# Optimization experiments

Measured on AMD Instinct MI355X. Metric: run time of the kernel, lower is better.

The kernel has to match this reference:

```python
import jax, jax.numpy as jnp
import numpy as np

N, E, D, H = 100000, 1600000, 128, 4
HD = D // H  # per-head dim


def setup_inputs() -> dict:
    key = jax.random.key(0)
    ks = jax.random.split(key, 16)
    s = 1.0 / np.sqrt(D)
    inp = {
        "x": jax.random.normal(ks[0], (N, D), jnp.float32),
        "edge_index": jax.random.randint(ks[1], (2, E), 0, N, jnp.int64),
        # GCNConv params
        "w_gcn": jax.random.normal(ks[2], (D, D), jnp.float32) * s,
        "b_gcn": jnp.zeros((D,), jnp.float32),
        # TransformerConv params (lin_query/key/value, lin_skip, lin_beta)
        "w_q": jax.random.normal(ks[3], (D, D), jnp.float32) * s,
        "b_q": jnp.zeros((D,), jnp.float32),
        "w_k": jax.random.normal(ks[4], (D, D), jnp.float32) * s,
        "b_k": jnp.zeros((D,), jnp.float32),
        "w_v": jax.random.normal(ks[5], (D, D), jnp.float32) * s,
        "b_v": jnp.zeros((D,), jnp.float32),
        "w_skip": jax.random.normal(ks[6], (D, D), jnp.float32) * s,
        "b_skip": jnp.zeros((D,), jnp.float32),
        "w_beta": jax.random.normal(ks[7], (3 * D, 1), jnp.float32) * s,
        # LayerNorms
        "ln1_g": jnp.ones((D,), jnp.float32),
        "ln1_b": jnp.zeros((D,), jnp.float32),
        "ln2_g": jnp.ones((D,), jnp.float32),
        "ln2_b": jnp.zeros((D,), jnp.float32),
        # FFN
        "w1": jax.random.normal(ks[8], (D, 2 * D), jnp.float32) * s,
        "b1": jnp.zeros((2 * D,), jnp.float32),
        "w2": jax.random.normal(ks[9], (2 * D, D), jnp.float32) * (1.0 / np.sqrt(2 * D)),
        "b2": jnp.zeros((D,), jnp.float32),
        "local_weight": jnp.ones((1,), jnp.float32),
        "global_weight": jnp.ones((1,), jnp.float32),
    }
    return inp


def _layer_norm(x, g, b, eps=1e-5):
    mu = jnp.mean(x, axis=-1, keepdims=True)
    var = jnp.var(x, axis=-1, keepdims=True)
    return (x - mu) * jax.lax.rsqrt(var + eps) * g + b


def _gps_forward(x, edge_index, w_gcn, b_gcn, w_q, b_q, w_k, b_k, w_v, b_v,
                 w_skip, b_skip, w_beta, ln1_g, ln1_b, ln2_g, ln2_b,
                 w1, b1, w2, b2, local_weight, global_weight):
    src, dst = edge_index[0], edge_index[1]  # messages flow src -> dst

    # ---- GCNConv (add_self_loops=False), sym norm ----
    deg = jax.ops.segment_sum(jnp.ones((E,), x.dtype), dst, num_segments=N)
    dinv = jnp.where(deg > 0, jax.lax.rsqrt(jnp.maximum(deg, 1.0)), 0.0)
    norm = dinv[src] * dinv[dst]  # [E]
    h = x @ w_gcn  # [N, D]
    local_out = jax.ops.segment_sum(h[src] * norm[:, None], dst, num_segments=N) + b_gcn

    # ---- TransformerConv (heads=H, concat=True, beta=True) ----
    q = (x @ w_q + b_q).reshape(N, H, HD)
    k = (x @ w_k + b_k).reshape(N, H, HD)
    v = (x @ w_v + b_v).reshape(N, H, HD)
    scores = jnp.sum(q[dst] * k[src], axis=-1) / np.sqrt(HD)  # [E, H]
    m = jax.ops.segment_max(scores, dst, num_segments=N)      # [N, H]
    m = jnp.where(jnp.isfinite(m), m, 0.0)
    e = jnp.exp(scores - m[dst])                              # [E, H]
    denom = jax.ops.segment_sum(e, dst, num_segments=N)       # [N, H]
    alpha = e / denom[dst]                                    # [E, H]
    agg = jax.ops.segment_sum(v[src] * alpha[:, :, None], dst, num_segments=N)
    out_attn = agg.reshape(N, D)
    x_r = x @ w_skip + b_skip
    beta = jax.nn.sigmoid(
        jnp.concatenate([out_attn, x_r, out_attn - x_r], axis=-1) @ w_beta)  # [N,1]
    global_out = beta * x_r + (1.0 - beta) * out_attn

    # ---- combine + LN + FFN + LN ----
    xc = local_weight * local_out + global_weight * global_out
    xn = _layer_norm(xc + xc, ln1_g, ln1_b)
    ff = jnp.maximum(xn @ w1 + b1, 0.0) @ w2 + b2
    return _layer_norm(ff + xn, ln2_g, ln2_b)


def reference(x, edge_index, w_gcn, b_gcn, w_q, b_q, w_k, b_k, w_v, b_v,
              w_skip, b_skip, w_beta, ln1_g, ln1_b, ln2_g, ln2_b,
              w1, b1, w2, b2, local_weight, global_weight):
    return _gps_forward(x, edge_index, w_gcn, b_gcn, w_q, b_q, w_k, b_k, w_v, b_v,
                        w_skip, b_skip, w_beta, ln1_g, ln1_b, ln2_g, ln2_b,
                        w1, b1, w2, b2, local_weight, global_weight)
```

## Files before the change

### kernel.cpp

```cpp
#include <hip/hip_runtime.h>

typedef unsigned int u32;
typedef unsigned short u16;
typedef __attribute__((ext_vector_type(8))) short bf16x8;
typedef __attribute__((ext_vector_type(4))) float f32x4;

__device__ __forceinline__ float bf2f(u16 u){ return __uint_as_float(((u32)u) << 16); }
__device__ __forceinline__ u16 f2bf(float f){
  u32 x = __float_as_uint(f);
  return (u16)((x + 0x7fffu + ((x >> 16) & 1u)) >> 16);
}

__global__ void k_prep_all(const float* wq, const float* bq, const float* wsk, const float* bsk,
                           const float* wk, const float* bk, const float* wv, const float* bv,
                           const float* wg, const float* w1, const float* w2,
                           u16* WcatT, float* bcat, u16* w1T, u16* w2T){
  int idx = blockIdx.x * 256 + threadIdx.x;
  if (idx < 640 * 128){
    int col = idx >> 7, k = idx & 127;
    int blk = col >> 7, c = col & 127;
    const float* w = (blk==0)?wq:(blk==1)?wsk:(blk==2)?wk:(blk==3)?wv:wg;
    WcatT[idx] = f2bf(w[k * 128 + c]);
    if (k == 0){
      const float* b = (blk==0)?bq:(blk==1)?bsk:(blk==2)?bk:(blk==3)?bv:nullptr;
      bcat[col] = b ? b[c] : 0.0f;
    }
  } else if (idx < 640*128 + 256*128){
    int j = idx - 640*128; int c = j >> 7, k = j & 127;
    w1T[j] = f2bf(w1[k * 256 + c]);
  } else if (idx < 640*128 + 256*128 + 128*256){
    int j = idx - (640*128 + 256*128); int c = j >> 8, k = j & 255;
    w2T[j] = f2bf(w2[k * 128 + c]);
  }
}

__global__ void k_cvt(const float* __restrict__ x, u16* __restrict__ xB, int n){
  int i = (blockIdx.x * 256 + threadIdx.x) * 4;
  if (i >= n) return;
  float4 v = *(const float4*)(x + i);
  ushort4 o; o.x = f2bf(v.x); o.y = f2bf(v.y); o.z = f2bf(v.z); o.w = f2bf(v.w);
  *(ushort4*)(xB + i) = o;
}

__global__ void k_hist(const int* __restrict__ ei, int E, int* __restrict__ deg){
  int e = blockIdx.x * 256 + threadIdx.x;
  if (e >= E) return;
  atomicAdd(&deg[ei[E + e]], 1);
}
__global__ void k_scan_a(const int* __restrict__ deg, int N, int* __restrict__ bsum){
  __shared__ int sh[256];
  int b = blockIdx.x, t = threadIdx.x;
  int base = b * 1024 + t * 4, s = 0;
  #pragma unroll
  for (int j = 0; j < 4; j++){ int i = base + j; if (i < N) s += deg[i]; }
  sh[t] = s; __syncthreads();
  for (int off = 128; off > 0; off >>= 1){ if (t < off) sh[t] += sh[t + off]; __syncthreads(); }
  if (t == 0) bsum[b] = sh[0];
}
__global__ void k_scan_b(const int* __restrict__ bsum, int NB, int* __restrict__ boff){
  __shared__ int sh[1024];
  int t = threadIdx.x;
  int self = (t < NB) ? bsum[t] : 0;
  sh[t] = self; __syncthreads();
  for (int off = 1; off < 1024; off <<= 1){
    int v = sh[t]; int add = (t >= off) ? sh[t - off] : 0;
    __syncthreads(); sh[t] = v + add; __syncthreads();
  }
  if (t < NB) boff[t] = sh[t] - self;
}
__global__ void k_scan_c(const int* __restrict__ deg, int N, int E,
                         const int* __restrict__ boff, int* __restrict__ rowptr){
  __shared__ int sh[256];
  int b = blockIdx.x, t = threadIdx.x;
  int base = b * 1024 + t * 4;
  int d[4]; int ts = 0;
  #pragma unroll
  for (int j = 0; j < 4; j++){ int i = base + j; d[j] = (i < N) ? deg[i] : 0; ts += d[j]; }
  sh[t] = ts; __syncthreads();
  for (int off = 1; off < 256; off <<= 1){
    int v = sh[t]; int add = (t >= off) ? sh[t - off] : 0;
    __syncthreads(); sh[t] = v + add; __syncthreads();
  }
  int excl = sh[t] - ts + boff[b];
  #pragma unroll
  for (int j = 0; j < 4; j++){ int i = base + j; if (i < N) rowptr[i] = excl; excl += d[j]; }
  if (b == 0 && t == 0) rowptr[N] = E;
}
__global__ void k_dinv(const int* __restrict__ deg, int N, float* __restrict__ dinv){
  int i = blockIdx.x * 256 + threadIdx.x;
  if (i < N) dinv[i] = deg[i] > 0 ? rsqrtf((float)deg[i]) : 0.0f;
}
__global__ void k_csr(const int* __restrict__ ei, int E,
                      const int* __restrict__ rowptr, int* __restrict__ fill, int* __restrict__ csr){
  int e = blockIdx.x * 256 + threadIdx.x;
  if (e >= E) return;
  int d = ei[E + e];
  int pos = rowptr[d] + atomicAdd(&fill[d], 1);
  csr[pos] = ei[e];
}

__device__ __forceinline__ void stageTile(const u16* __restrict__ g, int ldg, int row0, int rclamp,
                                          int kofs, u16* lds){
  int t = threadIdx.x;
  #pragma unroll
  for (int p = 0; p < 8; p++){
    int chunk = p * 256 + t;
    int r = chunk >> 4;
    int cs = (chunk & 15) << 3;
    int rg = row0 + r; if (rg >= rclamp) rg = rclamp - 1;
    bf16x8 v = *(const bf16x8*)(g + (size_t)rg * ldg + kofs + cs);
    *(bf16x8*)(lds + r * 128 + (cs ^ ((r & 7) << 3))) = v;
  }
}
__device__ __forceinline__ bf16x8 ldFrag(const u16* lds, int r, int k0){
  return *(const bf16x8*)(lds + r * 128 + (k0 ^ ((r & 7) << 3)));
}

__global__ __launch_bounds__(256) void k_gemm1(const u16* __restrict__ xB, const u16* __restrict__ WcatT,
    const float* __restrict__ bcat, u16* __restrict__ qB, u16* __restrict__ xrB,
    u16* __restrict__ kvhB, int N){
  __shared__ u16 As[128 * 128];
  __shared__ u16 Bs[128 * 128];
  int row0 = blockIdx.x * 128, cb = blockIdx.y;
  stageTile(xB, 128, row0, N, 0, As);
  stageTile(WcatT, 128, cb * 128, 1 << 30, 0, Bs);
  __syncthreads();
  int t = threadIdx.x, l = t & 63, w = t >> 6;
  int wm = w >> 1, wn = w & 1;
  int c16 = l & 15, g = l >> 4;
  f32x4 acc[4][4];
  #pragma unroll
  for (int mi = 0; mi < 4; mi++)
    #pragma unroll
    for (int ni = 0; ni < 4; ni++) acc[mi][ni] = (f32x4){0.f, 0.f, 0.f, 0.f};
  #pragma unroll
  for (int kk = 0; kk < 4; kk++){
    int k0 = kk * 32 + g * 8;
    bf16x8 af[4], bfr[4];
    #pragma unroll
    for (int mi = 0; mi < 4; mi++) af[mi] = ldFrag(As, wm * 64 + mi * 16 + c16, k0);
    #pragma unroll
    for (int ni = 0; ni < 4; ni++) bfr[ni] = ldFrag(Bs, wn * 64 + ni * 16 + c16, k0);
    #pragma unroll
    for (int mi = 0; mi < 4; mi++)
      #pragma unroll
      for (int ni = 0; ni < 4; ni++)
        acc[mi][ni] = __builtin_amdgcn_mfma_f32_16x16x32_bf16(af[mi], bfr[ni], acc[mi][ni], 0, 0, 0);
  }
  u16* dst; int ld, cofs;
  if (cb == 0){ dst = qB;  ld = 128; cofs = 0; }
  else if (cb == 1){ dst = xrB; ld = 128; cofs = 0; }
  else { dst = kvhB; ld = 384; cofs = (cb - 2) * 128; }
  float bias[4];
  #pragma unroll
  for (int ni = 0; ni < 4; ni++) bias[ni] = bcat[cb * 128 + wn * 64 + ni * 16 + c16];
  #pragma unroll
  for (int mi = 0; mi < 4; mi++){
    #pragma unroll
    for (int r = 0; r < 4; r++){
      int row = row0 + wm * 64 + mi * 16 + g * 4 + r;
      if (row < N){
        #pragma unroll
        for (int ni = 0; ni < 4; ni++)
          dst[(size_t)row * ld + cofs + wn * 64 + ni * 16 + c16] = f2bf(acc[mi][ni][r] + bias[ni]);
      }
    }
  }
}

__global__ __launch_bounds__(256) void k_edge(const u16* __restrict__ qB, const u16* __restrict__ xrB,
    const u16* __restrict__ kvhB,
    const int* __restrict__ csr, const int* __restrict__ rowptr, const float* __restrict__ dinv,
    const float* __restrict__ bgcn, const float* __restrict__ wbeta,
    const float* __restrict__ lng, const float* __restrict__ lnb,
    const float* __restrict__ lwp, const float* __restrict__ gwp,
    float* __restrict__ xn, u16* __restrict__ xnB, int N){
  int lane = threadIdx.x & 63;
  int n = blockIdx.x * 4 + (threadIdx.x >> 6);
  if (n >= N) return;
  int ro = rowptr[n], re = rowptr[n + 1];
  u32 qu = *(const u32*)(qB + (size_t)n * 128 + 2 * lane);
  float q0 = bf2f((u16)(qu & 0xffff)), q1 = bf2f((u16)(qu >> 16));
  float av0 = 0, av1 = 0, ah0 = 0, ah1 = 0, den = 0;
  int sNext = (ro < re) ? csr[ro] : 0;
  for (int e = ro; e < re; e++){
    int s = sNext;
    if (e + 1 < re) sNext = csr[e + 1];
    const u16* fb = kvhB + (size_t)s * 384;
    u32 ku = *(const u32*)(fb + 2 * lane);
    u32 vu = *(const u32*)(fb + 128 + 2 * lane);
    u32 hu = *(const u32*)(fb + 256 + 2 * lane);
    float dv = dinv[s];
    float k0 = bf2f((u16)(ku & 0xffff)), k1 = bf2f((u16)(ku >> 16));
    float part = q0 * k0 + q1 * k1;
    part += __shfl_xor(part, 1);
    part += __shfl_xor(part, 2);
    part += __shfl_xor(part, 4);
    part += __shfl_xor(part, 8);
    float p = __expf(part * 0.17677669529663687f);
    float v0 = bf2f((u16)(vu & 0xffff)), v1 = bf2f((u16)(vu >> 16));
    float h0 = bf2f((u16)(hu & 0xffff)), h1 = bf2f((u16)(hu >> 16));
    av0 += p * v0; av1 += p * v1;
    ah0 += dv * h0; ah1 += dv * h1;
    den += p;
  }
  float at0 = den > 0 ? av0 / den : 0.0f;
  float at1 = den > 0 ? av1 / den : 0.0f;
  u32 xru = *(const u32*)(xrB + (size_t)n * 128 + 2 * lane);
  float xr0 = bf2f((u16)(xru & 0xffff)), xr1 = bf2f((u16)(xru >> 16));
  float z = at0 * wbeta[2*lane] + at1 * wbeta[2*lane+1]
          + xr0 * wbeta[128 + 2*lane] + xr1 * wbeta[129 + 2*lane]
          + (at0 - xr0) * wbeta[256 + 2*lane] + (at1 - xr1) * wbeta[257 + 2*lane];
  z += __shfl_xor(z, 1); z += __shfl_xor(z, 2); z += __shfl_xor(z, 4);
  z += __shfl_xor(z, 8); z += __shfl_xor(z, 16); z += __shfl_xor(z, 32);
  float beta = 1.0f / (1.0f + __expf(-z));
  float dn = dinv[n];
  float l0 = dn * ah0 + bgcn[2*lane], l1 = dn * ah1 + bgcn[2*lane+1];
  float g0 = beta * xr0 + (1.0f - beta) * at0;
  float g1v = beta * xr1 + (1.0f - beta) * at1;
  float lw = lwp[0], gw = gwp[0];
  float t0 = 2.0f * (lw * l0 + gw * g0);
  float t1 = 2.0f * (lw * l1 + gw * g1v);
  float s = t0 + t1, sq = t0 * t0 + t1 * t1;
  s += __shfl_xor(s, 1);  sq += __shfl_xor(sq, 1);
  s += __shfl_xor(s, 2);  sq += __shfl_xor(sq, 2);
  s += __shfl_xor(s, 4);  sq += __shfl_xor(sq, 4);
  s += __shfl_xor(s, 8);  sq += __shfl_xor(sq, 8);
  s += __shfl_xor(s, 16); sq += __shfl_xor(sq, 16);
  s += __shfl_xor(s, 32); sq += __shfl_xor(sq, 32);
  float mu = s * (1.0f / 128.0f);
  float var = sq * (1.0f / 128.0f) - mu * mu;
  float inv = rsqrtf(var + 1e-5f);
  float o0 = (t0 - mu) * inv * lng[2*lane] + lnb[2*lane];
  float o1 = (t1 - mu) * inv * lng[2*lane+1] + lnb[2*lane+1];
  *(float2*)(xn + (size_t)n * 128 + 2 * lane) = make_float2(o0, o1);
  u32 pk = (u32)f2bf(o0) | ((u32)f2bf(o1) << 16);
  *(u32*)(xnB + (size_t)n * 128 + 2 * lane) = pk;
}

__global__ __launch_bounds__(256) void k_ffn1(const u16* __restrict__ xnB, const u16* __restrict__ w1T,
    const float* __restrict__ b1, u16* __restrict__ hid, int N){
  __shared__ u16 As[128 * 128];
  __shared__ u16 Bs[128 * 128];
  int row0 = blockIdx.x * 128, cb = blockIdx.y;
  stageTile(xnB, 128, row0, N, 0, As);
  stageTile(w1T, 128, cb * 128, 1 << 30, 0, Bs);
  __syncthreads();
  int t = threadIdx.x, l = t & 63, w = t >> 6;
  int wm = w >> 1, wn = w & 1;
  int c16 = l & 15, g = l >> 4;
  f32x4 acc[4][4];
  #pragma unroll
  for (int mi = 0; mi < 4; mi++)
    #pragma unroll
    for (int ni = 0; ni < 4; ni++) acc[mi][ni] = (f32x4){0.f, 0.f, 0.f, 0.f};
  #pragma unroll
  for (int kk = 0; kk < 4; kk++){
    int k0 = kk * 32 + g * 8;
    bf16x8 af[4], bfr[4];
    #pragma unroll
    for (int mi = 0; mi < 4; mi++) af[mi] = ldFrag(As, wm * 64 + mi * 16 + c16, k0);
    #pragma unroll
    for (int ni = 0; ni < 4; ni++) bfr[ni] = ldFrag(Bs, wn * 64 + ni * 16 + c16, k0);
    #pragma unroll
    for (int mi = 0; mi < 4; mi++)
      #pragma unroll
      for (int ni = 0; ni < 4; ni++)
        acc[mi][ni] = __builtin_amdgcn_mfma_f32_16x16x32_bf16(af[mi], bfr[ni], acc[mi][ni], 0, 0, 0);
  }
  float bias[4];
  #pragma unroll
  for (int ni = 0; ni < 4; ni++) bias[ni] = b1[cb * 128 + wn * 64 + ni * 16 + c16];
  #pragma unroll
  for (int mi = 0; mi < 4; mi++){
    #pragma unroll
    for (int r = 0; r < 4; r++){
      int row = row0 + wm * 64 + mi * 16 + g * 4 + r;
      if (row < N){
        #pragma unroll
        for (int ni = 0; ni < 4; ni++)
          hid[(size_t)row * 256 + cb * 128 + wn * 64 + ni * 16 + c16] =
              f2bf(fmaxf(acc[mi][ni][r] + bias[ni], 0.0f));
      }
    }
  }
}

__global__ __launch_bounds__(256) void k_ffn2(const u16* __restrict__ hid, const u16* __restrict__ w2T,
    const float* __restrict__ b2, const float* __restrict__ xnf,
    const float* __restrict__ g2, const float* __restrict__ bt2,
    float* __restrict__ out, int N){
  __shared__ u16 As[128 * 128];
  __shared__ u16 Bs[128 * 128];
  int row0 = blockIdx.x * 128;
  int t = threadIdx.x, l = t & 63, w = t >> 6;
  int c16 = l & 15, g = l >> 4;
  f32x4 acc[2][8];
  #pragma unroll
  for (int mi = 0; mi < 2; mi++)
    #pragma unroll
    for (int ni = 0; ni < 8; ni++) acc[mi][ni] = (f32x4){0.f, 0.f, 0.f, 0.f};
  for (int kc = 0; kc < 2; kc++){
    if (kc) __syncthreads();
    stageTile(hid, 256, row0, N, kc * 128, As);
    stageTile(w2T, 256, 0, 1 << 30, kc * 128, Bs);
    __syncthreads();
    #pragma unroll
    for (int kk = 0; kk < 4; kk++){
      int k0 = kk * 32 + g * 8;
      bf16x8 af[2], bfr[8];
      #pragma unroll
      for (int mi = 0; mi < 2; mi++) af[mi] = ldFrag(As, w * 32 + mi * 16 + c16, k0);
      #pragma unroll
      for (int ni = 0; ni < 8; ni++) bfr[ni] = ldFrag(Bs, ni * 16 + c16, k0);
      #pragma unroll
      for (int mi = 0; mi < 2; mi++)
        #pragma unroll
        for (int ni = 0; ni < 8; ni++)
          acc[mi][ni] = __builtin_amdgcn_mfma_f32_16x16x32_bf16(af[mi], bfr[ni], acc[mi][ni], 0, 0, 0);
    }
  }
  float b2c[8], g2c[8], btc[8];
  #pragma unroll
  for (int ni = 0; ni < 8; ni++){
    int col = ni * 16 + c16;
    b2c[ni] = b2[col]; g2c[ni] = g2[col]; btc[ni] = bt2[col];
  }
  #pragma unroll
  for (int mi = 0; mi < 2; mi++){
    #pragma unroll
    for (int r = 0; r < 4; r++){
      int row = row0 + w * 32 + mi * 16 + g * 4 + r;
      int rc = row < N ? row : N - 1;
      float z[8]; float s = 0.f, sq = 0.f;
      #pragma unroll
      for (int ni = 0; ni < 8; ni++){
        z[ni] = acc[mi][ni][r] + b2c[ni] + xnf[(size_t)rc * 128 + ni * 16 + c16];
        s += z[ni]; sq += z[ni] * z[ni];
      }
      s += __shfl_xor(s, 1); sq += __shfl_xor(sq, 1);
      s += __shfl_xor(s, 2); sq += __shfl_xor(sq, 2);
      s += __shfl_xor(s, 4); sq += __shfl_xor(sq, 4);
      s += __shfl_xor(s, 8); sq += __shfl_xor(sq, 8);
      float mu = s * (1.0f / 128.0f);
      float var = sq * (1.0f / 128.0f) - mu * mu;
      float inv = rsqrtf(var + 1e-5f);
      if (row < N){
        #pragma unroll
        for (int ni = 0; ni < 8; ni++)
          out[(size_t)row * 128 + ni * 16 + c16] = (z[ni] - mu) * inv * g2c[ni] + btc[ni];
      }
    }
  }
}

extern "C" void kernel_launch(void* const* d_in, const int* in_sizes, int n_in,
                              void* d_out, int out_size, void* d_ws, size_t ws_size,
                              hipStream_t stream){
  const float* x      = (const float*)d_in[0];
  const int*   ei     = (const int*)d_in[1];
  const float* w_gcn  = (const float*)d_in[2];
  const float* b_gcn  = (const float*)d_in[3];
  const float* w_q    = (const float*)d_in[4];
  const float* b_q    = (const float*)d_in[5];
  const float* w_k    = (const float*)d_in[6];
  const float* b_k    = (const float*)d_in[7];
  const float* w_v    = (const float*)d_in[8];
  const float* b_v    = (const float*)d_in[9];
  const float* w_skip = (const float*)d_in[10];
  const float* b_skip = (const float*)d_in[11];
  const float* w_beta = (const float*)d_in[12];
  const float* ln1_g  = (const float*)d_in[13];
  const float* ln1_b  = (const float*)d_in[14];
  const float* ln2_g  = (const float*)d_in[15];
  const float* ln2_b  = (const float*)d_in[16];
  const float* w1     = (const float*)d_in[17];
  const float* b1     = (const float*)d_in[18];
  const float* w2     = (const float*)d_in[19];
  const float* b2     = (const float*)d_in[20];
  const float* lw     = (const float*)d_in[21];
  const float* gw     = (const float*)d_in[22];
  int N = in_sizes[0] / 128;
  int E = in_sizes[1] / 2;
  float* outf = (float*)d_out;
  float* xn   = (float*)d_out;

  char* ws = (char*)d_ws;
  size_t off = 0;
  auto alloc = [&](size_t bytes) -> char* {
    char* p = ws + off; off += (bytes + 255) & ~(size_t)255; return p;
  };
  u16* kvhB   = (u16*)alloc((size_t)N * 384 * 2);
  u16* xrB    = (u16*)alloc((size_t)N * 128 * 2);
  u16* qB     = (u16*)alloc((size_t)N * 128 * 2);
  u16* xB     = (u16*)alloc((size_t)N * 128 * 2);
  int* csr    = (int*)alloc((size_t)E * 4);
  int* deg    = (int*)alloc((size_t)N * 4);
  int* rowptr = (int*)alloc((size_t)(N + 1) * 4);
  int* fill   = (int*)alloc((size_t)N * 4);
  float* dinv = (float*)alloc((size_t)N * 4);
  int NB = (N + 1023) >> 10;
  int* bsum   = (int*)alloc((size_t)NB * 4);
  int* boff   = (int*)alloc((size_t)NB * 4);
  u16* WcatT  = (u16*)alloc((size_t)640 * 128 * 2);
  float* bcat = (float*)alloc((size_t)640 * 4);
  u16* w1T    = (u16*)alloc((size_t)256 * 128 * 2);
  u16* w2T    = (u16*)alloc((size_t)128 * 256 * 2);
  u16* hid    = kvhB;
  u16* xnB    = xB;

  if (off > ws_size) return;

  hipMemsetAsync(deg, 0, (size_t)N * 4, stream);
  hipMemsetAsync(fill, 0, (size_t)N * 4, stream);

  k_prep_all<<<576, 256, 0, stream>>>(w_q, b_q, w_skip, b_skip, w_k, b_k, w_v, b_v, w_gcn,
                                      w1, w2, WcatT, bcat, w1T, w2T);
  k_cvt<<<(N * 128 / 4 + 255) / 256, 256, 0, stream>>>(x, xB, N * 128);
  k_hist<<<(E + 255) / 256, 256, 0, stream>>>(ei, E, deg);
  k_scan_a<<<NB, 256, 0, stream>>>(deg, N, bsum);
  k_scan_b<<<1, 1024, 0, stream>>>(bsum, NB, boff);
  k_scan_c<<<NB, 256, 0, stream>>>(deg, N, E, boff, rowptr);
  k_dinv<<<(N + 255) / 256, 256, 0, stream>>>(deg, N, dinv);
  k_csr<<<(E + 255) / 256, 256, 0, stream>>>(ei, E, rowptr, fill, csr);

  int MB = (N + 127) / 128;
  dim3 g1(MB, 5);
  k_gemm1<<<g1, 256, 0, stream>>>(xB, WcatT, bcat, qB, xrB, kvhB, N);
  k_edge<<<(N + 3) / 4, 256, 0, stream>>>(qB, xrB, kvhB, csr, rowptr, dinv, b_gcn, w_beta,
                                          ln1_g, ln1_b, lw, gw, xn, xnB, N);
  dim3 f1(MB, 2);
  k_ffn1<<<f1, 256, 0, stream>>>(xnB, w1T, b1, hid, N);
  k_ffn2<<<MB, 256, 0, stream>>>(hid, w2T, b2, xn, ln2_g, ln2_b, outf, N);
}
```

Before: 477.9 us.

## Split edge loop across wave halves with 4-wide feature vectors per lane

The per-node edge kernel now has each half of the 64-lane wave process alternate edges, with each lane handling 4 features through 8-byte loads instead of 2 features through 4-byte loads. The two halves' partial attention, value and GCN accumulators are combined with a cross-half shuffle, and only the first half writes the output. The aim is to double memory-level parallelism over the serial edge loop and widen gathers. The trade-off is extra shuffles, idle lanes in the epilogue, and dropping the csr prefetch.

```diff
diff --git a/kernel.cpp b/kernel.cpp
--- a/kernel.cpp
+++ b/kernel.cpp
@@ -6,6 +6,8 @@
 typedef __attribute__((ext_vector_type(4))) float f32x4;
 
 __device__ __forceinline__ float bf2f(u16 u){ return __uint_as_float(((u32)u) << 16); }
+__device__ __forceinline__ float bf2f_lo(u32 u){ return __uint_as_float(u << 16); }
+__device__ __forceinline__ float bf2f_hi(u32 u){ return __uint_as_float(u & 0xffff0000u); }
 __device__ __forceinline__ u16 f2bf(float f){
   u32 x = __float_as_uint(f);
   return (u16)((x + 0x7fffu + ((x >> 16) & 1u)) >> 16);
@@ -176,66 +178,88 @@
     const float* __restrict__ lwp, const float* __restrict__ gwp,
     float* __restrict__ xn, u16* __restrict__ xnB, int N){
   int lane = threadIdx.x & 63;
+  int half = lane >> 5;
+  int li = lane & 31;
+  int d0 = li * 4;
   int n = blockIdx.x * 4 + (threadIdx.x >> 6);
   if (n >= N) return;
   int ro = rowptr[n], re = rowptr[n + 1];
-  u32 qu = *(const u32*)(qB + (size_t)n * 128 + 2 * lane);
-  float q0 = bf2f((u16)(qu & 0xffff)), q1 = bf2f((u16)(qu >> 16));
-  float av0 = 0, av1 = 0, ah0 = 0, ah1 = 0, den = 0;
-  int sNext = (ro < re) ? csr[ro] : 0;
-  for (int e = ro; e < re; e++){
-    int s = sNext;
-    if (e + 1 < re) sNext = csr[e + 1];
+  uint2 qu = *(const uint2*)(qB + (size_t)n * 128 + d0);
+  float q0 = bf2f_lo(qu.x), q1 = bf2f_hi(qu.x), q2 = bf2f_lo(qu.y), q3 = bf2f_hi(qu.y);
+  float av0 = 0, av1 = 0, av2 = 0, av3 = 0;
+  float ah0 = 0, ah1 = 0, ah2 = 0, ah3 = 0;
+  float den = 0;
+  const float SC = 0.17677669529663687f;
+  for (int e = ro + half; e < re; e += 2){
+    int s = csr[e];
     const u16* fb = kvhB + (size_t)s * 384;
-    u32 ku = *(const u32*)(fb + 2 * lane);
-    u32 vu = *(const u32*)(fb + 128 + 2 * lane);
-    u32 hu = *(const u32*)(fb + 256 + 2 * lane);
+    uint2 ku = *(const uint2*)(fb + d0);
+    uint2 vu = *(const uint2*)(fb + 128 + d0);
+    uint2 hu = *(const uint2*)(fb + 256 + d0);
     float dv = dinv[s];
-    float k0 = bf2f((u16)(ku & 0xffff)), k1 = bf2f((u16)(ku >> 16));
-    float part = q0 * k0 + q1 * k1;
+    float part = q0 * bf2f_lo(ku.x) + q1 * bf2f_hi(ku.x)
+               + q2 * bf2f_lo(ku.y) + q3 * bf2f_hi(ku.y);
     part += __shfl_xor(part, 1);
     part += __shfl_xor(part, 2);
     part += __shfl_xor(part, 4);
-    part += __shfl_xor(part, 8);
-    float p = __expf(part * 0.17677669529663687f);
-    float v0 = bf2f((u16)(vu & 0xffff)), v1 = bf2f((u16)(vu >> 16));
-    float h0 = bf2f((u16)(hu & 0xffff)), h1 = bf2f((u16)(hu >> 16));
-    av0 += p * v0; av1 += p * v1;
-    ah0 += dv * h0; ah1 += dv * h1;
+    float p = __expf(part * SC);
+    av0 += p * bf2f_lo(vu.x); av1 += p * bf2f_hi(vu.x);
+    av2 += p * bf2f_lo(vu.y); av3 += p * bf2f_hi(vu.y);
+    ah0 += dv * bf2f_lo(hu.x); ah1 += dv * bf2f_hi(hu.x);
+    ah2 += dv * bf2f_lo(hu.y); ah3 += dv * bf2f_hi(hu.y);
     den += p;
   }
-  float at0 = den > 0 ? av0 / den : 0.0f;
-  float at1 = den > 0 ? av1 / den : 0.0f;
-  u32 xru = *(const u32*)(xrB + (size_t)n * 128 + 2 * lane);
-  float xr0 = bf2f((u16)(xru & 0xffff)), xr1 = bf2f((u16)(xru >> 16));
-  float z = at0 * wbeta[2*lane] + at1 * wbeta[2*lane+1]
-          + xr0 * wbeta[128 + 2*lane] + xr1 * wbeta[129 + 2*lane]
-          + (at0 - xr0) * wbeta[256 + 2*lane] + (at1 - xr1) * wbeta[257 + 2*lane];
+  den += __shfl_xor(den, 32);
+  av0 += __shfl_xor(av0, 32); av1 += __shfl_xor(av1, 32);
+  av2 += __shfl_xor(av2, 32); av3 += __shfl_xor(av3, 32);
+  ah0 += __shfl_xor(ah0, 32); ah1 += __shfl_xor(ah1, 32);
+  ah2 += __shfl_xor(ah2, 32); ah3 += __shfl_xor(ah3, 32);
+  float inv_den = den > 0 ? 1.0f / den : 0.0f;
+  float at0 = av0 * inv_den, at1 = av1 * inv_den, at2 = av2 * inv_den, at3 = av3 * inv_den;
+  uint2 xru = *(const uint2*)(xrB + (size_t)n * 128 + d0);
+  float xr0 = bf2f_lo(xru.x), xr1 = bf2f_hi(xru.x), xr2 = bf2f_lo(xru.y), xr3 = bf2f_hi(xru.y);
+  float4 wb0 = *(const float4*)(wbeta + d0);
+  float4 wb1 = *(const float4*)(wbeta + 128 + d0);
+  float4 wb2 = *(const float4*)(wbeta + 256 + d0);
+  float z = at0 * wb0.x + at1 * wb0.y + at2 * wb0.z + at3 * wb0.w
+          + xr0 * wb1.x + xr1 * wb1.y + xr2 * wb1.z + xr3 * wb1.w
+          + (at0 - xr0) * wb2.x + (at1 - xr1) * wb2.y
+          + (at2 - xr2) * wb2.z + (at3 - xr3) * wb2.w;
   z += __shfl_xor(z, 1); z += __shfl_xor(z, 2); z += __shfl_xor(z, 4);
-  z += __shfl_xor(z, 8); z += __shfl_xor(z, 16); z += __shfl_xor(z, 32);
+  z += __shfl_xor(z, 8); z += __shfl_xor(z, 16);
   float beta = 1.0f / (1.0f + __expf(-z));
   float dn = dinv[n];
-  float l0 = dn * ah0 + bgcn[2*lane], l1 = dn * ah1 + bgcn[2*lane+1];
-  float g0 = beta * xr0 + (1.0f - beta) * at0;
-  float g1v = beta * xr1 + (1.0f - beta) * at1;
+  float4 bg = *(const float4*)(bgcn + d0);
+  float l0 = dn * ah0 + bg.x, l1 = dn * ah1 + bg.y, l2 = dn * ah2 + bg.z, l3 = dn * ah3 + bg.w;
   float lw = lwp[0], gw = gwp[0];
-  float t0 = 2.0f * (lw * l0 + gw * g0);
-  float t1 = 2.0f * (lw * l1 + gw * g1v);
-  float s = t0 + t1, sq = t0 * t0 + t1 * t1;
+  float ib = 1.0f - beta;
+  float t0 = 2.0f * (lw * l0 + gw * (beta * xr0 + ib * at0));
+  float t1 = 2.0f * (lw * l1 + gw * (beta * xr1 + ib * at1));
+  float t2 = 2.0f * (lw * l2 + gw * (beta * xr2 + ib * at2));
+  float t3 = 2.0f * (lw * l3 + gw * (beta * xr3 + ib * at3));
+  float s = t0 + t1 + t2 + t3;
+  float sq = t0*t0 + t1*t1 + t2*t2 + t3*t3;
   s += __shfl_xor(s, 1);  sq += __shfl_xor(sq, 1);
   s += __shfl_xor(s, 2);  sq += __shfl_xor(sq, 2);
   s += __shfl_xor(s, 4);  sq += __shfl_xor(sq, 4);
   s += __shfl_xor(s, 8);  sq += __shfl_xor(sq, 8);
   s += __shfl_xor(s, 16); sq += __shfl_xor(sq, 16);
-  s += __shfl_xor(s, 32); sq += __shfl_xor(sq, 32);
   float mu = s * (1.0f / 128.0f);
   float var = sq * (1.0f / 128.0f) - mu * mu;
   float inv = rsqrtf(var + 1e-5f);
-  float o0 = (t0 - mu) * inv * lng[2*lane] + lnb[2*lane];
-  float o1 = (t1 - mu) * inv * lng[2*lane+1] + lnb[2*lane+1];
-  *(float2*)(xn + (size_t)n * 128 + 2 * lane) = make_float2(o0, o1);
-  u32 pk = (u32)f2bf(o0) | ((u32)f2bf(o1) << 16);
-  *(u32*)(xnB + (size_t)n * 128 + 2 * lane) = pk;
+  if (half == 0){
+    float4 gm = *(const float4*)(lng + d0);
+    float4 bt = *(const float4*)(lnb + d0);
+    float o0 = (t0 - mu) * inv * gm.x + bt.x;
+    float o1 = (t1 - mu) * inv * gm.y + bt.y;
+    float o2 = (t2 - mu) * inv * gm.z + bt.z;
+    float o3 = (t3 - mu) * inv * gm.w + bt.w;
+    *(float4*)(xn + (size_t)n * 128 + d0) = make_float4(o0, o1, o2, o3);
+    uint2 pk;
+    pk.x = (u32)f2bf(o0) | ((u32)f2bf(o1) << 16);
+    pk.y = (u32)f2bf(o2) | ((u32)f2bf(o3) << 16);
+    *(uint2*)(xnB + (size_t)n * 128 + d0) = pk;
+  }
 }
 
 __global__ __launch_bounds__(256) void k_ffn1(const u16* __restrict__ xnB, const u16* __restrict__ w1T,
```

After: 472.7 us. No clear change (-1.1%).
